# Kernel optimization log

Measured on AMD Instinct MI355X. Metric: run time of the kernel, lower is better.

Reference implementation:

```python
import jax, jax.numpy as jnp
import numpy as np

GROUPS = 32
EPS = 1e-5


def group_norm(x, scale, bias):
    b, c, h, w = x.shape
    xg = x.reshape(b, GROUPS, c // GROUPS, h, w)
    mean = jnp.mean(xg, axis=(2, 3, 4), keepdims=True)
    var = jnp.var(xg, axis=(2, 3, 4), keepdims=True)
    xn = (xg - mean) * jax.lax.rsqrt(var + EPS)
    xn = xn.reshape(b, c, h, w)
    return xn * scale[None, :, None, None] + bias[None, :, None, None]


def conv1x1(x, w, b):
    # x: [b,c,h,w], w: [out,in] -> [b,out,h,w]
    return jnp.einsum('bchw,oc->bohw', x, w) + b[None, :, None, None]


def setup_inputs() -> dict:
    key = jax.random.key(0)
    ks = jax.random.split(key, 8)
    B, C, H, W = 4, 512, 64, 64
    s = 1.0 / np.sqrt(C)
    return {
        'x': jax.random.normal(ks[0], (B, C, H, W), jnp.float32),
        'norm_scale': jnp.ones((C,), jnp.float32),
        'norm_bias': jnp.zeros((C,), jnp.float32),
        'wq': jax.random.normal(ks[1], (C, C), jnp.float32) * s,
        'bq': jnp.zeros((C,), jnp.float32),
        'wk': jax.random.normal(ks[2], (C, C), jnp.float32) * s,
        'bk': jnp.zeros((C,), jnp.float32),
        'wv': jax.random.normal(ks[3], (C, C), jnp.float32) * s,
        'bv': jnp.zeros((C,), jnp.float32),
        'wo': jax.random.normal(ks[4], (C, C), jnp.float32) * s,
        'bo': jnp.zeros((C,), jnp.float32),
    }


def reference(x, norm_scale, norm_bias, wq, bq, wk, bk, wv, bv, wo, bo):
    b, c, h, w = x.shape
    hn = group_norm(x, norm_scale, norm_bias)
    q = conv1x1(hn, wq, bq)  # [b,c,h,w]
    k = conv1x1(hn, wk, bk)
    v = conv1x1(hn, wv, bv)
    n = h * w
    q = q.reshape(b, c, n).transpose(0, 2, 1)  # [b,n,c]
    k = k.reshape(b, c, n)                     # [b,c,n]
    v = v.reshape(b, c, n).transpose(0, 2, 1)  # [b,n,c]
    scale = jnp.asarray(c, x.dtype) ** -0.5
    attn = jax.nn.softmax(jnp.einsum('bic,bcj->bij', q, k) * scale, axis=-1)
    out = jnp.einsum('bij,bjc->bic', attn, v)  # [b,n,c]
    out = out.transpose(0, 2, 1).reshape(b, c, h, w)
    return x + conv1x1(out, wo, bo)
```

## Files before the change

### kernel.cpp

```cpp
#include <hip/hip_runtime.h>
#include <math.h>

#define B_ 4
#define C_ 512
#define N_ 4096
#define NG 32

typedef __attribute__((ext_vector_type(4))) float f32x4;
typedef __attribute__((ext_vector_type(8))) short bf16x8;
typedef __attribute__((ext_vector_type(8))) unsigned short u16x8;
typedef __attribute__((ext_vector_type(4))) unsigned short u16x4;

__device__ __forceinline__ unsigned short f2bf(float f){
  unsigned u = __float_as_uint(f);
  return (unsigned short)((u + 0x7fffu + ((u >> 16) & 1u)) >> 16);
}
__device__ __forceinline__ float bf2f(unsigned short h){
  return __uint_as_float(((unsigned)h) << 16);
}

__global__ __launch_bounds__(256) void gn_stats_k(const float* __restrict__ x, float* __restrict__ stats){
  int bg = blockIdx.x;
  const float4* xp = (const float4*)(x + (size_t)bg * 65536);
  float s = 0.f, ss = 0.f;
  for (int i = threadIdx.x; i < 16384; i += 256){
    float4 v = xp[i];
    s  += v.x + v.y + v.z + v.w;
    ss += v.x*v.x + v.y*v.y + v.z*v.z + v.w*v.w;
  }
  __shared__ float ls[256], lq[256];
  ls[threadIdx.x] = s; lq[threadIdx.x] = ss;
  __syncthreads();
  for (int o = 128; o > 0; o >>= 1){
    if (threadIdx.x < o){ ls[threadIdx.x] += ls[threadIdx.x+o]; lq[threadIdx.x] += lq[threadIdx.x+o]; }
    __syncthreads();
  }
  if (threadIdx.x == 0){
    float mean = ls[0] * (1.f/65536.f);
    float var  = lq[0] * (1.f/65536.f) - mean*mean;
    stats[bg*2+0] = mean;
    stats[bg*2+1] = rsqrtf(var + 1e-5f);
  }
}

__global__ __launch_bounds__(256) void gn_apply_k(const float* __restrict__ x, const float* __restrict__ stats,
    const float* __restrict__ gam, const float* __restrict__ bet, unsigned short* __restrict__ hn){
  __shared__ unsigned short tile[C_][33];
  int b = blockIdx.y, n0 = blockIdx.x * 32;
  const float* xb = x + (size_t)b * C_ * N_;
  for (int i = threadIdx.x; i < 4096; i += 256){
    int c = i >> 3, j4 = (i & 7) * 4;
    float4 v = *(const float4*)(xb + (size_t)c * N_ + n0 + j4);
    int g = c >> 4;
    float mean = stats[(b*NG+g)*2], rstd = stats[(b*NG+g)*2+1];
    float sc = gam[c] * rstd;
    float bi = bet[c] - mean * sc;
    tile[c][j4+0] = f2bf(v.x*sc+bi);
    tile[c][j4+1] = f2bf(v.y*sc+bi);
    tile[c][j4+2] = f2bf(v.z*sc+bi);
    tile[c][j4+3] = f2bf(v.w*sc+bi);
  }
  __syncthreads();
  for (int i = threadIdx.x; i < 2048; i += 256){
    int cc = (i & 63) * 8, j = i >> 6;
    u16x8 o;
    #pragma unroll
    for (int t = 0; t < 8; t++) o[t] = tile[cc+t][j];
    *(u16x8*)(hn + ((size_t)b*N_ + n0 + j) * C_ + cc) = o;
  }
}

__global__ __launch_bounds__(256) void prep_w_k(const float* __restrict__ wq, const float* __restrict__ wk,
    const float* __restrict__ wv, const float* __restrict__ wo,
    unsigned short* __restrict__ wqkv, unsigned short* __restrict__ wob, float scl){
  int i = blockIdx.x * 256 + threadIdx.x;
  int mat = i >> 16, idx = i & 65535;
  const float* src = (mat==0) ? wq : (mat==1) ? wk : (mat==2) ? wv : wo;
  float s = (mat==0) ? scl : 1.f;
  float4 v = ((const float4*)src)[idx];
  u16x4 o; o[0]=f2bf(v.x*s); o[1]=f2bf(v.y*s); o[2]=f2bf(v.z*s); o[3]=f2bf(v.w*s);
  if (mat < 3) ((u16x4*)wqkv)[mat*65536 + idx] = o;
  else         ((u16x4*)wob)[idx] = o;
}

__global__ __launch_bounds__(256) void prep_b_k(const float* __restrict__ bq, const float* __restrict__ bk,
    const float* __restrict__ bv, float* __restrict__ bqkv, float scl){
  int i = blockIdx.x * 256 + threadIdx.x;
  if (i < 512) bqkv[i] = bq[i] * scl;
  else if (i < 1024) bqkv[i] = bk[i-512];
  else if (i < 1536) bqkv[i] = bv[i-1024];
}

template<int BIAS_MODE , bool OUT_BF16, bool RESID>
__global__ __launch_bounds__(512) void gemm_bt_k(
    const unsigned short* __restrict__ A, const unsigned short* __restrict__ Bt,
    void* __restrict__ Cv, const float* __restrict__ bias, const float* __restrict__ resid,
    int Ncols, int K, int lda, int ldb,
    long long sA, long long sB, long long sC, long long sR, float scale)
{
  const int tid = threadIdx.x;
  const int bz = blockIdx.z;
  A  += (size_t)bz * sA;
  Bt += (size_t)bz * sB;

  const int nwg = gridDim.x * gridDim.y;
  const int wg  = blockIdx.y * gridDim.x + blockIdx.x;
  const int swz = (wg & 7) * (nwg >> 3) + (wg >> 3);
  const int bx = swz % gridDim.x, by = swz / gridDim.x;

  const int tn = bx * 128, tm = by * 256;
  __shared__ unsigned short lA[2][256*32];
  __shared__ unsigned short lB[2][128*32];
  const int wave = tid >> 6, lane = tid & 63;
  const int wm = (wave >> 1) * 64, wn = (wave & 1) * 64;
  f32x4 acc[4][4] = {};

  const unsigned short* Abase = A + (size_t)tm * lda;
  const unsigned short* Bbase = Bt + (size_t)tn * ldb;

  const int srow = tid >> 2, pch = tid & 3;
  const int sch  = pch ^ ((srow >> 1) & 3);
  const size_t aoff0 = (size_t)srow       * lda + sch*8;
  const size_t aoff1 = (size_t)(srow+128) * lda + sch*8;
  const size_t boff0 = (size_t)srow       * ldb + sch*8;
  const int ldst0 = srow*32       + pch*8;
  const int ldst1 = (srow+128)*32 + pch*8;

  auto issue = [&](int buf, int k0){
    __builtin_amdgcn_global_load_lds((const __attribute__((address_space(1))) unsigned int*)(Abase + aoff0 + k0),
        (__attribute__((address_space(3))) unsigned int*)(&lA[buf][ldst0]), 16, 0, 0);
    __builtin_amdgcn_global_load_lds((const __attribute__((address_space(1))) unsigned int*)(Abase + aoff1 + k0),
        (__attribute__((address_space(3))) unsigned int*)(&lA[buf][ldst1]), 16, 0, 0);
    __builtin_amdgcn_global_load_lds((const __attribute__((address_space(1))) unsigned int*)(Bbase + boff0 + k0),
        (__attribute__((address_space(3))) unsigned int*)(&lB[buf][ldst0]), 16, 0, 0);
  };

  issue(0, 0);
  __syncthreads();
  const int T = K >> 5;
  for (int t = 0; t < T; t++){
    const int cur = t & 1;
    if (t + 1 < T) issue(cur ^ 1, (t + 1) << 5);

    bf16x8 af[4], bfb[4];
    const int lr = lane & 15, q = lane >> 4;
    #pragma unroll
    for (int i = 0; i < 4; i++){
      int row = wm + i*16 + lr;
      af[i]  = *(const bf16x8*)&lA[cur][row*32 + ((q ^ ((row >> 1) & 3)) * 8)];
    }
    #pragma unroll
    for (int j = 0; j < 4; j++){
      int row = wn + j*16 + lr;
      bfb[j] = *(const bf16x8*)&lB[cur][row*32 + ((q ^ ((row >> 1) & 3)) * 8)];
    }
    #pragma unroll
    for (int i = 0; i < 4; i++)
      #pragma unroll
      for (int j = 0; j < 4; j++)
        acc[i][j] = __builtin_amdgcn_mfma_f32_16x16x32_bf16(af[i], bfb[j], acc[i][j], 0, 0, 0);

    __syncthreads();
  }

  const int rr = (lane >> 4) * 4, cl = lane & 15;
  #pragma unroll
  for (int i = 0; i < 4; i++){
    #pragma unroll
    for (int j = 0; j < 4; j++){
      int col = tn + wn + j*16 + cl;
      float cb = (BIAS_MODE == 1) ? bias[col] : 0.f;
      #pragma unroll
      for (int r = 0; r < 4; r++){
        int row = tm + wm + i*16 + rr + r;
        float v = acc[i][j][r];
        if (BIAS_MODE == 1) v += cb;
        if (BIAS_MODE == 2) v += bias[row];
        v *= scale;
        size_t idx = (size_t)bz * sC + (size_t)row * Ncols + col;
        if (RESID) v += resid[(size_t)bz * sR + (size_t)row * Ncols + col];
        if (OUT_BF16) ((unsigned short*)Cv)[idx] = f2bf(v);
        else          ((float*)Cv)[idx] = v;
      }
    }
  }
}

__global__ __launch_bounds__(256) void transpose_v_k(const unsigned short* __restrict__ QKV, unsigned short* __restrict__ Vt){
  __shared__ unsigned short t[64][72];
  int b = blockIdx.z, c0 = blockIdx.x * 64, n0 = blockIdx.y * 64;
  int tid = threadIdx.x;
  for (int i = tid; i < 512; i += 256){
    int n = i >> 3, cc = (i & 7) * 8;
    u16x8 v = *(const u16x8*)&QKV[((size_t)b*N_ + n0 + n)*1536 + 1024 + c0 + cc];
    #pragma unroll
    for (int j = 0; j < 8; j++) t[cc+j][n] = v[j];
  }
  __syncthreads();
  for (int i = tid; i < 512; i += 256){
    int c = i >> 3, nn = (i & 7) * 8;
    u16x8 o;
    #pragma unroll
    for (int j = 0; j < 8; j++) o[j] = t[c][nn+j];
    *(u16x8*)&Vt[((size_t)b*C_ + c0 + c)*N_ + n0 + nn] = o;
  }
}

__global__ __launch_bounds__(256) void softmax_k(unsigned short* __restrict__ SP){
  size_t row = blockIdx.x;
  u16x8* sp = (u16x8*)(SP + row * 4096);
  const int t = threadIdx.x;
  u16x8 h0 = sp[t], h1 = sp[t + 256];
  float v[16];
  #pragma unroll
  for (int j = 0; j < 8; j++){ v[j] = bf2f(h0[j]); v[8+j] = bf2f(h1[j]); }
  float m = -3.0e38f;
  #pragma unroll
  for (int j = 0; j < 16; j++) m = fmaxf(m, v[j]);
  #pragma unroll
  for (int o = 32; o > 0; o >>= 1) m = fmaxf(m, __shfl_xor(m, o));
  __shared__ float red[4], red2[4];
  if ((t & 63) == 0) red[t >> 6] = m;
  __syncthreads();
  m = fmaxf(fmaxf(red[0], red[1]), fmaxf(red[2], red[3]));
  float s = 0.f;
  #pragma unroll
  for (int j = 0; j < 16; j++){ float e = __expf(v[j] - m); v[j] = e; s += e; }
  #pragma unroll
  for (int o = 32; o > 0; o >>= 1) s += __shfl_xor(s, o);
  if ((t & 63) == 0) red2[t >> 6] = s;
  __syncthreads();
  s = red2[0] + red2[1] + red2[2] + red2[3];
  float inv = 1.0f / s;
  u16x8 o0, o1;
  #pragma unroll
  for (int j = 0; j < 8; j++){ o0[j] = f2bf(v[j] * inv); o1[j] = f2bf(v[8+j] * inv); }
  sp[t] = o0; sp[t + 256] = o1;
}

extern "C" void kernel_launch(void* const* d_in, const int* in_sizes, int n_in,
                              void* d_out, int out_size, void* d_ws, size_t ws_size,
                              hipStream_t stream)
{
  (void)in_sizes; (void)n_in; (void)out_size;
  const float* x   = (const float*)d_in[0];
  const float* gam = (const float*)d_in[1];
  const float* bet = (const float*)d_in[2];
  const float* wq  = (const float*)d_in[3];
  const float* bq  = (const float*)d_in[4];
  const float* wk  = (const float*)d_in[5];
  const float* bk  = (const float*)d_in[6];
  const float* wv  = (const float*)d_in[7];
  const float* bv  = (const float*)d_in[8];
  const float* wo  = (const float*)d_in[9];
  const float* bo  = (const float*)d_in[10];

  char* ws = (char*)d_ws;
  size_t off = 0;
  auto alloc = [&](size_t bytes)->void*{ void* p = ws + off; off += (bytes + 255) & ~(size_t)255; return p; };
  unsigned short* hn   = (unsigned short*)alloc((size_t)B_*N_*C_*2);
  unsigned short* QKV  = (unsigned short*)alloc((size_t)B_*N_*1536*2);
  unsigned short* Vt   = (unsigned short*)alloc((size_t)B_*C_*N_*2);
  unsigned short* O    = (unsigned short*)alloc((size_t)B_*N_*C_*2);
  unsigned short* wqkv = (unsigned short*)alloc((size_t)3*C_*C_*2);
  unsigned short* wob  = (unsigned short*)alloc((size_t)C_*C_*2);
  float* bqkv          = (float*)alloc(1536*4);
  float* stats         = (float*)alloc((size_t)B_*NG*2*4);

  size_t base = off;
  long long avail = (long long)ws_size - (long long)base;
  long long per_row = (long long)N_*2;
  long long rows_ll = avail > 0 ? avail / per_row : 0;
  int rows = (int)(rows_ll > 16384 ? 16384 : rows_ll);
  rows = (rows / 256) * 256;
  if (rows < 256) rows = 256;
  unsigned short* S = (unsigned short*)(ws + base);

  const float scl = 0.044194173824159216f;
  const long long NC  = (long long)N_ * C_;
  const long long CN  = (long long)C_ * N_;
  const long long NN  = (long long)N_ * N_;
  const long long NC3 = (long long)N_ * 1536;

  prep_w_k<<<dim3(1024), 256, 0, stream>>>(wq, wk, wv, wo, wqkv, wob, scl);
  prep_b_k<<<dim3(6),    256, 0, stream>>>(bq, bk, bv, bqkv, scl);

  gn_stats_k<<<dim3(B_*NG), 256, 0, stream>>>(x, stats);
  gn_apply_k<<<dim3(N_/32, B_), 256, 0, stream>>>(x, stats, gam, bet, hn);

  gemm_bt_k<1,true,false><<<dim3(1536/128, B_*N_/256, 1), 512, 0, stream>>>(
      hn, wqkv, QKV, bqkv, nullptr, 1536, C_, C_, C_, 0,0,0,0, 1.f);

  transpose_v_k<<<dim3(C_/64, N_/64, B_), 256, 0, stream>>>(QKV, Vt);

  if (rows >= B_*N_){
    gemm_bt_k<0,true,false><<<dim3(N_/128, N_/256, B_), 512, 0, stream>>>(
        QKV, QKV + 512, S, nullptr, nullptr, N_, C_, 1536, 1536, NC3, NC3, NN, 0, 1.f);
    softmax_k<<<dim3(B_*N_), 256, 0, stream>>>(S);
    gemm_bt_k<0,true,false><<<dim3(C_/128, N_/256, B_), 512, 0, stream>>>(
        S, Vt, O, nullptr, nullptr, C_, N_, N_, N_, NN, CN, NC, 0, 1.f);
  } else {
    int CH = rows > N_ ? N_ : rows;
    for (int b = 0; b < B_; b++){
      for (int r0 = 0; r0 < N_; r0 += CH){
        int ch = (N_ - r0) < CH ? (N_ - r0) : CH;
        gemm_bt_k<0,true,false><<<dim3(N_/128, ch/256, 1), 512, 0, stream>>>(
            QKV + ((size_t)b*N_ + r0)*1536, QKV + (size_t)b*N_*1536 + 512, S, nullptr, nullptr,
            N_, C_, 1536, 1536, 0,0,0,0, 1.f);
        softmax_k<<<dim3(ch), 256, 0, stream>>>(S);
        gemm_bt_k<0,true,false><<<dim3(C_/128, ch/256, 1), 512, 0, stream>>>(
            S, Vt + (size_t)b*C_*N_, O + ((size_t)b*N_ + r0)*C_, nullptr, nullptr,
            C_, N_, N_, N_, 0,0,0,0, 1.f);
      }
    }
  }

  gemm_bt_k<2,false,true><<<dim3(N_/128, C_/256, B_), 512, 0, stream>>>(
      wob, O, (float*)d_out, bo, x, N_, C_, C_, C_, 0, NC, CN, CN, 1.f);
}
```

Before: 340.2 us.

## Deepen GEMM LDS pipeline to four stages with explicit vmcnt waits

```diff
diff --git a/kernel.cpp b/kernel.cpp
--- a/kernel.cpp
+++ b/kernel.cpp
@@ -109,8 +109,8 @@
   const int bx = swz % gridDim.x, by = swz / gridDim.x;
 
   const int tn = bx * 128, tm = by * 256;
-  __shared__ unsigned short lA[2][256*32];
-  __shared__ unsigned short lB[2][128*32];
+  __shared__ unsigned short lA[4][256*32];
+  __shared__ unsigned short lB[4][128*32];
   const int wave = tid >> 6, lane = tid & 63;
   const int wm = (wave >> 1) * 64, wn = (wave & 1) * 64;
   f32x4 acc[4][4] = {};
@@ -126,41 +126,53 @@
   const int ldst0 = srow*32       + pch*8;
   const int ldst1 = (srow+128)*32 + pch*8;
 
-  auto issue = [&](int buf, int k0){
+  auto issue = [&](int slot, int k0){
     __builtin_amdgcn_global_load_lds((const __attribute__((address_space(1))) unsigned int*)(Abase + aoff0 + k0),
-        (__attribute__((address_space(3))) unsigned int*)(&lA[buf][ldst0]), 16, 0, 0);
+        (__attribute__((address_space(3))) unsigned int*)(&lA[slot][ldst0]), 16, 0, 0);
     __builtin_amdgcn_global_load_lds((const __attribute__((address_space(1))) unsigned int*)(Abase + aoff1 + k0),
-        (__attribute__((address_space(3))) unsigned int*)(&lA[buf][ldst1]), 16, 0, 0);
+        (__attribute__((address_space(3))) unsigned int*)(&lA[slot][ldst1]), 16, 0, 0);
     __builtin_amdgcn_global_load_lds((const __attribute__((address_space(1))) unsigned int*)(Bbase + boff0 + k0),
-        (__attribute__((address_space(3))) unsigned int*)(&lB[buf][ldst0]), 16, 0, 0);
+        (__attribute__((address_space(3))) unsigned int*)(&lB[slot][ldst0]), 16, 0, 0);
   };
 
+  const int T = K >> 5;
   issue(0, 0);
-  __syncthreads();
-  const int T = K >> 5;
+  if (T > 1) issue(1, 32);
+  if (T > 2) issue(2, 64);
+
   for (int t = 0; t < T; t++){
-    const int cur = t & 1;
-    if (t + 1 < T) issue(cur ^ 1, (t + 1) << 5);
+    const int slot = t & 3;
+    if (t + 3 <= T)      { asm volatile("s_waitcnt vmcnt(6)" ::: "memory"); }
+    else if (t == T - 2) { asm volatile("s_waitcnt vmcnt(3)" ::: "memory"); }
+    else                 { asm volatile("s_waitcnt vmcnt(0)" ::: "memory"); }
+    __builtin_amdgcn_sched_barrier(0);
+    __builtin_amdgcn_s_barrier();
+    __builtin_amdgcn_sched_barrier(0);
+
+    if (t + 3 < T) issue((t + 3) & 3, (t + 3) << 5);
 
     bf16x8 af[4], bfb[4];
     const int lr = lane & 15, q = lane >> 4;
     #pragma unroll
     for (int i = 0; i < 4; i++){
       int row = wm + i*16 + lr;
-      af[i]  = *(const bf16x8*)&lA[cur][row*32 + ((q ^ ((row >> 1) & 3)) * 8)];
+      af[i]  = *(const bf16x8*)&lA[slot][row*32 + ((q ^ ((row >> 1) & 3)) * 8)];
     }
     #pragma unroll
     for (int j = 0; j < 4; j++){
       int row = wn + j*16 + lr;
-      bfb[j] = *(const bf16x8*)&lB[cur][row*32 + ((q ^ ((row >> 1) & 3)) * 8)];
+      bfb[j] = *(const bf16x8*)&lB[slot][row*32 + ((q ^ ((row >> 1) & 3)) * 8)];
     }
+    __builtin_amdgcn_s_setprio(1);
     #pragma unroll
     for (int i = 0; i < 4; i++)
       #pragma unroll
       for (int j = 0; j < 4; j++)
         acc[i][j] = __builtin_amdgcn_mfma_f32_16x16x32_bf16(af[i], bfb[j], acc[i][j], 0, 0, 0);
-
-    __syncthreads();
+    __builtin_amdgcn_s_setprio(0);
+
+    asm volatile("s_waitcnt lgkmcnt(0)" ::: "memory");
+    __builtin_amdgcn_sched_barrier(0);
   }
 
   const int rr = (lane >> 4) * 4, cl = lane & 15;
```

Result: slower. 405.9 us (+19.3%).

## Fuse softmax into QK and PV GEMMs via per-tile row statistics

Applied to the files above, without the earlier changes.

```diff
diff --git a/kernel.cpp b/kernel.cpp
--- a/kernel.cpp
+++ b/kernel.cpp
@@ -91,12 +91,27 @@
   else if (i < 1536) bqkv[i] = bv[i-1024];
 }
 
-template<int BIAS_MODE , bool OUT_BF16, bool RESID>
+__global__ __launch_bounds__(256) void sm_stats_k(const float2* __restrict__ part,
+    float* __restrict__ mrow, float* __restrict__ rsum){
+  int i = blockIdx.x * 256 + threadIdx.x;
+  const float2* p = part + (size_t)i * 64;
+  float M = -3.0e38f;
+  #pragma unroll 4
+  for (int j = 0; j < 64; j++) M = fmaxf(M, p[j].x);
+  float S = 0.f;
+  #pragma unroll 4
+  for (int j = 0; j < 64; j++) S += p[j].y * __expf(p[j].x - M);
+  mrow[i] = M;
+  rsum[i] = 1.f / S;
+}
+
+template<int BIAS_MODE , bool OUT_BF16, bool RESID, bool STATS, bool FUSE>
 __global__ __launch_bounds__(512) void gemm_bt_k(
     const unsigned short* __restrict__ A, const unsigned short* __restrict__ Bt,
     void* __restrict__ Cv, const float* __restrict__ bias, const float* __restrict__ resid,
     int Ncols, int K, int lda, int ldb,
-    long long sA, long long sB, long long sC, long long sR, float scale)
+    long long sA, long long sB, long long sC, long long sR, float scale,
+    float2* __restrict__ part, const float* __restrict__ mrow, const float* __restrict__ rsum)
 {
   const int tid = threadIdx.x;
   const int bz = blockIdx.z;
@@ -109,6 +124,7 @@
   const int bx = swz % gridDim.x, by = swz / gridDim.x;
 
   const int tn = bx * 128, tm = by * 256;
+  const int Mtot = gridDim.y * 256;
   __shared__ unsigned short lA[2][256*32];
   __shared__ unsigned short lB[2][128*32];
   const int wave = tid >> 6, lane = tid & 63;
@@ -126,21 +142,50 @@
   const int ldst0 = srow*32       + pch*8;
   const int ldst1 = (srow+128)*32 + pch*8;
 
-  auto issue = [&](int buf, int k0){
+  float m0 = 0.f, m1 = 0.f;
+  if (FUSE){
+    m0 = mrow[(size_t)bz * Mtot + tm + srow];
+    m1 = mrow[(size_t)bz * Mtot + tm + srow + 128];
+  }
+
+  auto issueA = [&](int buf, int k0){
     __builtin_amdgcn_global_load_lds((const __attribute__((address_space(1))) unsigned int*)(Abase + aoff0 + k0),
         (__attribute__((address_space(3))) unsigned int*)(&lA[buf][ldst0]), 16, 0, 0);
     __builtin_amdgcn_global_load_lds((const __attribute__((address_space(1))) unsigned int*)(Abase + aoff1 + k0),
         (__attribute__((address_space(3))) unsigned int*)(&lA[buf][ldst1]), 16, 0, 0);
+  };
+  auto issueB = [&](int buf, int k0){
     __builtin_amdgcn_global_load_lds((const __attribute__((address_space(1))) unsigned int*)(Bbase + boff0 + k0),
         (__attribute__((address_space(3))) unsigned int*)(&lB[buf][ldst0]), 16, 0, 0);
   };
 
-  issue(0, 0);
-  __syncthreads();
+  u16x8 a0, a1;
+  auto loadA = [&](int k0){
+    a0 = *(const u16x8*)(Abase + aoff0 + k0);
+    a1 = *(const u16x8*)(Abase + aoff1 + k0);
+  };
+  auto writeA = [&](int buf){
+    u16x8 p0, p1;
+    #pragma unroll
+    for (int j = 0; j < 8; j++){
+      p0[j] = f2bf(__expf(bf2f(a0[j]) - m0));
+      p1[j] = f2bf(__expf(bf2f(a1[j]) - m1));
+    }
+    *(u16x8*)&lA[buf][ldst0] = p0;
+    *(u16x8*)&lA[buf][ldst1] = p1;
+  };
+
+  if (FUSE){ loadA(0); issueB(0, 0); writeA(0); }
+  else     { issueA(0, 0); issueB(0, 0); }
+  __syncthreads();
+
   const int T = K >> 5;
   for (int t = 0; t < T; t++){
     const int cur = t & 1;
-    if (t + 1 < T) issue(cur ^ 1, (t + 1) << 5);
+    if (t + 1 < T){
+      if (FUSE){ loadA((t + 1) << 5); issueB(cur ^ 1, (t + 1) << 5); }
+      else     { issueA(cur ^ 1, (t + 1) << 5); issueB(cur ^ 1, (t + 1) << 5); }
+    }
 
     bf16x8 af[4], bfb[4];
     const int lr = lane & 15, q = lane >> 4;
@@ -159,6 +204,8 @@
       #pragma unroll
       for (int j = 0; j < 4; j++)
         acc[i][j] = __builtin_amdgcn_mfma_f32_16x16x32_bf16(af[i], bfb[j], acc[i][j], 0, 0, 0);
+
+    if (FUSE && t + 1 < T) writeA(cur ^ 1);
 
     __syncthreads();
   }
@@ -177,10 +224,35 @@
         if (BIAS_MODE == 1) v += cb;
         if (BIAS_MODE == 2) v += bias[row];
         v *= scale;
+        if (FUSE) v *= rsum[(size_t)bz * Mtot + row];
         size_t idx = (size_t)bz * sC + (size_t)row * Ncols + col;
         if (RESID) v += resid[(size_t)bz * sR + (size_t)row * Ncols + col];
         if (OUT_BF16) ((unsigned short*)Cv)[idx] = f2bf(v);
         else          ((float*)Cv)[idx] = v;
+      }
+    }
+  }
+
+  if (STATS){
+    #pragma unroll
+    for (int i = 0; i < 4; i++){
+      #pragma unroll
+      for (int r = 0; r < 4; r++){
+        float vr[4];
+        float mx = -3.0e38f;
+        #pragma unroll
+        for (int j = 0; j < 4; j++){ vr[j] = bf2f(f2bf(acc[i][j][r])); mx = fmaxf(mx, vr[j]); }
+        #pragma unroll
+        for (int o = 1; o < 16; o <<= 1) mx = fmaxf(mx, __shfl_xor(mx, o));
+        float se = 0.f;
+        #pragma unroll
+        for (int j = 0; j < 4; j++) se += __expf(vr[j] - mx);
+        #pragma unroll
+        for (int o = 1; o < 16; o <<= 1) se += __shfl_xor(se, o);
+        if ((lane & 15) == 0){
+          int row = tm + wm + i*16 + rr + r;
+          part[((size_t)bz * Mtot + row) * 64 + bx*2 + (wave & 1)] = make_float2(mx, se);
+        }
       }
     }
   }
@@ -266,6 +338,9 @@
   unsigned short* wob  = (unsigned short*)alloc((size_t)C_*C_*2);
   float* bqkv          = (float*)alloc(1536*4);
   float* stats         = (float*)alloc((size_t)B_*NG*2*4);
+  float2* part         = (float2*)alloc((size_t)B_*N_*64*8);
+  float* mrowb         = (float*)alloc((size_t)B_*N_*4);
+  float* rsumb         = (float*)alloc((size_t)B_*N_*4);
 
   size_t base = off;
   long long avail = (long long)ws_size - (long long)base;
@@ -288,33 +363,35 @@
   gn_stats_k<<<dim3(B_*NG), 256, 0, stream>>>(x, stats);
   gn_apply_k<<<dim3(N_/32, B_), 256, 0, stream>>>(x, stats, gam, bet, hn);
 
-  gemm_bt_k<1,true,false><<<dim3(1536/128, B_*N_/256, 1), 512, 0, stream>>>(
-      hn, wqkv, QKV, bqkv, nullptr, 1536, C_, C_, C_, 0,0,0,0, 1.f);
+  gemm_bt_k<1,true,false,false,false><<<dim3(1536/128, B_*N_/256, 1), 512, 0, stream>>>(
+      hn, wqkv, QKV, bqkv, nullptr, 1536, C_, C_, C_, 0,0,0,0, 1.f, nullptr, nullptr, nullptr);
 
   transpose_v_k<<<dim3(C_/64, N_/64, B_), 256, 0, stream>>>(QKV, Vt);
 
   if (rows >= B_*N_){
-    gemm_bt_k<0,true,false><<<dim3(N_/128, N_/256, B_), 512, 0, stream>>>(
-        QKV, QKV + 512, S, nullptr, nullptr, N_, C_, 1536, 1536, NC3, NC3, NN, 0, 1.f);
-    softmax_k<<<dim3(B_*N_), 256, 0, stream>>>(S);
-    gemm_bt_k<0,true,false><<<dim3(C_/128, N_/256, B_), 512, 0, stream>>>(
-        S, Vt, O, nullptr, nullptr, C_, N_, N_, N_, NN, CN, NC, 0, 1.f);
+    gemm_bt_k<0,true,false,true,false><<<dim3(N_/128, N_/256, B_), 512, 0, stream>>>(
+        QKV, QKV + 512, S, nullptr, nullptr, N_, C_, 1536, 1536, NC3, NC3, NN, 0, 1.f,
+        part, nullptr, nullptr);
+    sm_stats_k<<<dim3(B_*N_/256), 256, 0, stream>>>(part, mrowb, rsumb);
+    gemm_bt_k<0,true,false,false,true><<<dim3(C_/128, N_/256, B_), 512, 0, stream>>>(
+        S, Vt, O, nullptr, nullptr, C_, N_, N_, N_, NN, CN, NC, 0, 1.f,
+        nullptr, mrowb, rsumb);
   } else {
     int CH = rows > N_ ? N_ : rows;
     for (int b = 0; b < B_; b++){
       for (int r0 = 0; r0 < N_; r0 += CH){
         int ch = (N_ - r0) < CH ? (N_ - r0) : CH;
-        gemm_bt_k<0,true,false><<<dim3(N_/128, ch/256, 1), 512, 0, stream>>>(
+        gemm_bt_k<0,true,false,false,false><<<dim3(N_/128, ch/256, 1), 512, 0, stream>>>(
             QKV + ((size_t)b*N_ + r0)*1536, QKV + (size_t)b*N_*1536 + 512, S, nullptr, nullptr,
-            N_, C_, 1536, 1536, 0,0,0,0, 1.f);
+            N_, C_, 1536, 1536, 0,0,0,0, 1.f, nullptr, nullptr, nullptr);
         softmax_k<<<dim3(ch), 256, 0, stream>>>(S);
-        gemm_bt_k<0,true,false><<<dim3(C_/128, ch/256, 1), 512, 0, stream>>>(
+        gemm_bt_k<0,true,false,false,false><<<dim3(C_/128, ch/256, 1), 512, 0, stream>>>(
             S, Vt + (size_t)b*C_*N_, O + ((size_t)b*N_ + r0)*C_, nullptr, nullptr,
-            C_, N_, N_, N_, 0,0,0,0, 1.f);
+            C_, N_, N_, N_, 0,0,0,0, 1.f, nullptr, nullptr, nullptr);
       }
     }
   }
 
-  gemm_bt_k<2,false,true><<<dim3(N_/128, C_/256, B_), 512, 0, stream>>>(
-      wob, O, (float*)d_out, bo, x, N_, C_, C_, C_, 0, NC, CN, CN, 1.f);
-}
+  gemm_bt_k<2,false,true,false,false><<<dim3(N_/128, C_/256, B_), 512, 0, stream>>>(
+      wob, O, (float*)d_out, bo, x, N_, C_, C_, C_, 0, NC, CN, CN, 1.f, nullptr, nullptr, nullptr);
+}
```

Result: slower. 381.2 us (+12.1%).

## Fuse softmax exp and row-sum partials into QK GEMM epilogue, normalize in PV GEMM

Applied to the files above, without the earlier changes.

```diff
diff --git a/kernel.cpp b/kernel.cpp
--- a/kernel.cpp
+++ b/kernel.cpp
@@ -91,12 +91,22 @@
   else if (i < 1536) bqkv[i] = bv[i-1024];
 }
 
-template<int BIAS_MODE , bool OUT_BF16, bool RESID>
+__global__ __launch_bounds__(256) void sm_stats_k(const float* __restrict__ part, float* __restrict__ rsum){
+  int i = blockIdx.x * 256 + threadIdx.x;
+  const float4* p = (const float4*)(part + (size_t)i * 64);
+  float S = 0.f;
+  #pragma unroll
+  for (int j = 0; j < 16; j++){ float4 v = p[j]; S += v.x + v.y + v.z + v.w; }
+  rsum[i] = 1.f / S;
+}
+
+template<int BIAS_MODE , bool OUT_BF16, bool RESID, bool EXPSTATS, bool SCALE_ROW>
 __global__ __launch_bounds__(512) void gemm_bt_k(
     const unsigned short* __restrict__ A, const unsigned short* __restrict__ Bt,
     void* __restrict__ Cv, const float* __restrict__ bias, const float* __restrict__ resid,
     int Ncols, int K, int lda, int ldb,
-    long long sA, long long sB, long long sC, long long sR, float scale)
+    long long sA, long long sB, long long sC, long long sR, float scale,
+    float* __restrict__ part, const float* __restrict__ rsum)
 {
   const int tid = threadIdx.x;
   const int bz = blockIdx.z;
@@ -109,6 +119,7 @@
   const int bx = swz % gridDim.x, by = swz / gridDim.x;
 
   const int tn = bx * 128, tm = by * 256;
+  const int Mtot = gridDim.y * 256;
   __shared__ unsigned short lA[2][256*32];
   __shared__ unsigned short lB[2][128*32];
   const int wave = tid >> 6, lane = tid & 63;
@@ -167,20 +178,34 @@
   #pragma unroll
   for (int i = 0; i < 4; i++){
     #pragma unroll
-    for (int j = 0; j < 4; j++){
-      int col = tn + wn + j*16 + cl;
-      float cb = (BIAS_MODE == 1) ? bias[col] : 0.f;
+    for (int r = 0; r < 4; r++){
+      int row = tm + wm + i*16 + rr + r;
+      float se = 0.f;
       #pragma unroll
-      for (int r = 0; r < 4; r++){
-        int row = tm + wm + i*16 + rr + r;
+      for (int j = 0; j < 4; j++){
+        int col = tn + wn + j*16 + cl;
         float v = acc[i][j][r];
-        if (BIAS_MODE == 1) v += cb;
+        if (BIAS_MODE == 1) v += bias[col];
         if (BIAS_MODE == 2) v += bias[row];
         v *= scale;
+        if (SCALE_ROW) v *= rsum[(size_t)bz * Mtot + row];
         size_t idx = (size_t)bz * sC + (size_t)row * Ncols + col;
         if (RESID) v += resid[(size_t)bz * sR + (size_t)row * Ncols + col];
-        if (OUT_BF16) ((unsigned short*)Cv)[idx] = f2bf(v);
-        else          ((float*)Cv)[idx] = v;
+        if (EXPSTATS){
+          unsigned short h = f2bf(__expf(v));
+          ((unsigned short*)Cv)[idx] = h;
+          se += bf2f(h);
+        } else if (OUT_BF16){
+          ((unsigned short*)Cv)[idx] = f2bf(v);
+        } else {
+          ((float*)Cv)[idx] = v;
+        }
+      }
+      if (EXPSTATS){
+        #pragma unroll
+        for (int o = 1; o < 16; o <<= 1) se += __shfl_xor(se, o);
+        if ((lane & 15) == 0)
+          part[((size_t)bz * Mtot + row) * 64 + bx*2 + (wave & 1)] = se;
       }
     }
   }
@@ -266,6 +291,8 @@
   unsigned short* wob  = (unsigned short*)alloc((size_t)C_*C_*2);
   float* bqkv          = (float*)alloc(1536*4);
   float* stats         = (float*)alloc((size_t)B_*NG*2*4);
+  float* part          = (float*)alloc((size_t)B_*N_*64*4);
+  float* rsumb         = (float*)alloc((size_t)B_*N_*4);
 
   size_t base = off;
   long long avail = (long long)ws_size - (long long)base;
@@ -288,33 +315,35 @@
   gn_stats_k<<<dim3(B_*NG), 256, 0, stream>>>(x, stats);
   gn_apply_k<<<dim3(N_/32, B_), 256, 0, stream>>>(x, stats, gam, bet, hn);
 
-  gemm_bt_k<1,true,false><<<dim3(1536/128, B_*N_/256, 1), 512, 0, stream>>>(
-      hn, wqkv, QKV, bqkv, nullptr, 1536, C_, C_, C_, 0,0,0,0, 1.f);
+  gemm_bt_k<1,true,false,false,false><<<dim3(1536/128, B_*N_/256, 1), 512, 0, stream>>>(
+      hn, wqkv, QKV, bqkv, nullptr, 1536, C_, C_, C_, 0,0,0,0, 1.f, nullptr, nullptr);
 
   transpose_v_k<<<dim3(C_/64, N_/64, B_), 256, 0, stream>>>(QKV, Vt);
 
   if (rows >= B_*N_){
-    gemm_bt_k<0,true,false><<<dim3(N_/128, N_/256, B_), 512, 0, stream>>>(
-        QKV, QKV + 512, S, nullptr, nullptr, N_, C_, 1536, 1536, NC3, NC3, NN, 0, 1.f);
-    softmax_k<<<dim3(B_*N_), 256, 0, stream>>>(S);
-    gemm_bt_k<0,true,false><<<dim3(C_/128, N_/256, B_), 512, 0, stream>>>(
-        S, Vt, O, nullptr, nullptr, C_, N_, N_, N_, NN, CN, NC, 0, 1.f);
+    gemm_bt_k<0,true,false,true,false><<<dim3(N_/128, N_/256, B_), 512, 0, stream>>>(
+        QKV, QKV + 512, S, nullptr, nullptr, N_, C_, 1536, 1536, NC3, NC3, NN, 0, 1.f,
+        part, nullptr);
+    sm_stats_k<<<dim3(B_*N_/256), 256, 0, stream>>>(part, rsumb);
+    gemm_bt_k<0,true,false,false,true><<<dim3(C_/128, N_/256, B_), 512, 0, stream>>>(
+        S, Vt, O, nullptr, nullptr, C_, N_, N_, N_, NN, CN, NC, 0, 1.f,
+        nullptr, rsumb);
   } else {
     int CH = rows > N_ ? N_ : rows;
     for (int b = 0; b < B_; b++){
       for (int r0 = 0; r0 < N_; r0 += CH){
         int ch = (N_ - r0) < CH ? (N_ - r0) : CH;
-        gemm_bt_k<0,true,false><<<dim3(N_/128, ch/256, 1), 512, 0, stream>>>(
+        gemm_bt_k<0,true,false,false,false><<<dim3(N_/128, ch/256, 1), 512, 0, stream>>>(
             QKV + ((size_t)b*N_ + r0)*1536, QKV + (size_t)b*N_*1536 + 512, S, nullptr, nullptr,
-            N_, C_, 1536, 1536, 0,0,0,0, 1.f);
+            N_, C_, 1536, 1536, 0,0,0,0, 1.f, nullptr, nullptr);
         softmax_k<<<dim3(ch), 256, 0, stream>>>(S);
-        gemm_bt_k<0,true,false><<<dim3(C_/128, ch/256, 1), 512, 0, stream>>>(
+        gemm_bt_k<0,true,false,false,false><<<dim3(C_/128, ch/256, 1), 512, 0, stream>>>(
             S, Vt + (size_t)b*C_*N_, O + ((size_t)b*N_ + r0)*C_, nullptr, nullptr,
-            C_, N_, N_, N_, 0,0,0,0, 1.f);
+            C_, N_, N_, N_, 0,0,0,0, 1.f, nullptr, nullptr);
       }
     }
   }
 
-  gemm_bt_k<2,false,true><<<dim3(N_/128, C_/256, B_), 512, 0, stream>>>(
-      wob, O, (float*)d_out, bo, x, N_, C_, C_, C_, 0, NC, CN, CN, 1.f);
-}
+  gemm_bt_k<2,false,true,false,false><<<dim3(N_/128, C_/256, B_), 512, 0, stream>>>(
+      wob, O, (float*)d_out, bo, x, N_, C_, C_, C_, 0, NC, CN, CN, 1.f, nullptr, nullptr);
+}
```

After: 313.1 us. -8.0%, faster.
